# Optimization experiments

Hardware: AMD Instinct MI355X
Metric: run time of the kernel (lower is better)

## Reference

```python
import jax, jax.numpy as jnp
import numpy as np

# DCNV3_YOLO config: inc==ouc=128 (no stem_conv), k=3, s=1, pad=autopad(3)=1, g=4, d=1, SiLU act
N, C, H, W = 4, 128, 96, 96
G = 4
GC = C // G          # group channels = 32
K = 3                # dcn kernel (also depthwise conv kernel)
PAD = 1
P = K * K            # sampling points per group
EPS = 1e-5


def setup_inputs() -> dict:
    key = jax.random.key(0)
    ks = jax.random.split(key, 8)
    d = {}
    d["x"] = jax.random.normal(ks[0], (N, C, H, W), jnp.float32)
    # DCNv3 params (torch Linear weight (out,in) -> stored transposed (in,out) here)
    d["dw_w"] = jax.random.normal(ks[1], (C, 1, K, K), jnp.float32) * 0.1  # depthwise conv
    d["dw_b"] = jnp.zeros((C,), jnp.float32)
    d["ln_g"] = jnp.ones((C,), jnp.float32)   # LN inside dw_conv branch
    d["ln_b"] = jnp.zeros((C,), jnp.float32)
    d["w_off"] = jax.random.normal(ks[2], (C, G * P * 2), jnp.float32) * 0.01
    d["b_off"] = jnp.zeros((G * P * 2,), jnp.float32)
    d["w_mask"] = jax.random.normal(ks[3], (C, G * P), jnp.float32) * 0.02
    d["b_mask"] = jnp.zeros((G * P,), jnp.float32)
    d["w_in"] = jax.random.normal(ks[4], (C, C), jnp.float32) * (1.0 / np.sqrt(C))
    d["b_in"] = jnp.zeros((C,), jnp.float32)
    d["w_out"] = jax.random.normal(ks[5], (C, C), jnp.float32) * (1.0 / np.sqrt(C))
    d["b_out"] = jnp.zeros((C,), jnp.float32)
    # BatchNorm2d (eval mode: running stats)
    d["bn_g"] = jnp.ones((C,), jnp.float32)
    d["bn_b"] = jnp.zeros((C,), jnp.float32)
    d["bn_mean"] = jnp.zeros((C,), jnp.float32)
    d["bn_var"] = jnp.ones((C,), jnp.float32)
    return d


def _dcnv3_core(xp, offset, mask):
    # xp: (N,H,W,C) projected input; offset: (N,H,W,G*P*2); mask: (N,H,W,G,P) softmaxed
    n, h, w, _ = xp.shape
    xpad = jnp.pad(xp, ((0, 0), (PAD, PAD), (PAD, PAD), (0, 0)))
    H_in, W_in = h + 2 * PAD, w + 2 * PAD
    Ho, Wo = h, w  # stride 1, k=3, pad=1 -> same spatial size
    # reference points (pixel centers in padded frame, normalized), matches _get_reference_points
    base = (K - 1) // 2 + 0.5  # 1.5
    ref_y = (jnp.arange(Ho, dtype=jnp.float32) + base) / H_in
    ref_x = (jnp.arange(Wo, dtype=jnp.float32) + base) / W_in
    # dilation grid; torch flattens meshgrid(x_lin, y_lin) ij -> x outer, y inner
    lin = jnp.arange(K, dtype=jnp.float32) - (K - 1) // 2  # [-1,0,1]
    gx, gy = jnp.meshgrid(lin, lin, indexing='ij')  # (K,K), x varies along axis 0
    gridx = (gx / W_in).reshape(P)
    gridy = (gy / H_in).reshape(P)
    off = offset.reshape(n, Ho, Wo, G, P, 2)
    # normalized sampling locations (offset_scale = 1.0)
    loc_x = ref_x[None, None, :, None, None] + gridx[None, None, None, None, :] + off[..., 0] / W_in
    loc_y = ref_y[None, :, None, None, None] + gridy[None, None, None, None, :] + off[..., 1] / H_in
    # grid_sample(align_corners=False) unnormalize of (2*loc-1): loc*size - 0.5
    ix = (loc_x * W_in - 0.5).transpose(0, 3, 1, 2, 4)  # (N,G,Ho,Wo,P)
    iy = (loc_y * H_in - 0.5).transpose(0, 3, 1, 2, 4)
    x0 = jnp.floor(ix); y0 = jnp.floor(iy)
    wx1 = ix - x0; wx0 = 1.0 - wx1
    wy1 = iy - y0; wy0 = 1.0 - wy1
    x0i = x0.astype(jnp.int32); y0i = y0.astype(jnp.int32)
    x1i = x0i + 1; y1i = y0i + 1
    img = xpad.reshape(n, H_in * W_in, G, GC).transpose(0, 2, 1, 3)  # (N,G,S,GC)

    def samp(yi, xi, wgt):
        valid = (yi >= 0) & (yi < H_in) & (xi >= 0) & (xi < W_in)  # zeros padding
        idx = jnp.clip(yi, 0, H_in - 1) * W_in + jnp.clip(xi, 0, W_in - 1)
        idxf = idx.reshape(n, G, Ho * Wo * P, 1)
        v = jnp.take_along_axis(img, idxf, axis=2)  # (N,G,Ho*Wo*P,GC)
        w_eff = jnp.where(valid, wgt, 0.0).reshape(n, G, Ho * Wo * P, 1)
        return v * w_eff

    val = (samp(y0i, x0i, wy0 * wx0) + samp(y0i, x1i, wy0 * wx1)
           + samp(y1i, x0i, wy1 * wx0) + samp(y1i, x1i, wy1 * wx1))
    val = val.reshape(n, G, Ho, Wo, P, GC)
    m = mask.transpose(0, 3, 1, 2, 4)[..., None]  # (N,G,Ho,Wo,P,1)
    out = (val * m).sum(axis=4)  # (N,G,Ho,Wo,GC)
    return out.transpose(0, 2, 3, 1, 4).reshape(n, Ho, Wo, G * GC)


def reference(x, dw_w, dw_b, ln_g, ln_b, w_off, b_off, w_mask, b_mask,
              w_in, b_in, w_out, b_out, bn_g, bn_b, bn_mean, bn_var):
    x_nhwc = x.transpose(0, 2, 3, 1)  # NCHW -> NHWC
    x_proj = x_nhwc @ w_in + b_in     # input_proj
    # dw_conv branch: depthwise conv -> LayerNorm(channels_last) -> GELU
    x1 = jax.lax.conv_general_dilated(x, dw_w, (1, 1), ((PAD, PAD), (PAD, PAD)),
                                      feature_group_count=C,
                                      dimension_numbers=('NCHW', 'OIHW', 'NCHW'))
    x1 = x1.transpose(0, 2, 3, 1) + dw_b
    mu = x1.mean(-1, keepdims=True)
    var = ((x1 - mu) ** 2).mean(-1, keepdims=True)
    x1 = (x1 - mu) * jax.lax.rsqrt(var + EPS) * ln_g + ln_b
    x1 = jax.nn.gelu(x1, approximate=False)
    offset = x1 @ w_off + b_off  # (N,H,W,G*P*2)
    mask = jax.nn.softmax((x1 @ w_mask + b_mask).reshape(N, H, W, G, P), axis=-1)
    out = _dcnv3_core(x_proj, offset, mask)
    out = out @ w_out + b_out    # output_proj
    y = out.transpose(0, 3, 1, 2)  # back to NCHW
    # BatchNorm2d (eval) + SiLU
    inv = jax.lax.rsqrt(bn_var + EPS)
    y = (y - bn_mean[:, None, None]) * (inv * bn_g)[:, None, None] + bn_b[:, None, None]
    return y * jax.nn.sigmoid(y)
```

## Files before the change

### kernel.cpp

```cpp
#include <hip/hip_runtime.h>
#include <math.h>

#define NN 4
#define CCH 128
#define HH 96
#define WW 96
#define SS (HH*WW)
#define GG 4
#define GC 32
#define PP 9
#define NPIX (NN*HH*WW)

typedef short bf16x8 __attribute__((ext_vector_type(8)));
typedef float f32x4 __attribute__((ext_vector_type(4)));
typedef unsigned short u16;
typedef unsigned int u32;

static __device__ __forceinline__ u16 f2bf(float f) {
  unsigned u = __builtin_bit_cast(unsigned, f);
  unsigned r = (u + 0x7fffu + ((u >> 16) & 1u)) >> 16;
  return (u16)r;
}
static __device__ __forceinline__ float bflo(u32 u) {
  return __builtin_bit_cast(float, u << 16);
}
static __device__ __forceinline__ float bfhi(u32 u) {
  return __builtin_bit_cast(float, u & 0xffff0000u);
}

__global__ __launch_bounds__(128) void k_prep(const float* __restrict__ w_in,
    const float* __restrict__ w_off, const float* __restrict__ w_mask,
    const float* __restrict__ w_out, const float* __restrict__ dw_w,
    u16* __restrict__ w_inT, u16* __restrict__ w_omT, u16* __restrict__ w_outT,
    u16* __restrict__ dw_wT) {
  int r = blockIdx.x, k = threadIdx.x;
  if (r < 128) {
    w_inT[r*128 + k] = f2bf(w_in[k*128 + r]);
  } else if (r < 240) {
    int c = r - 128;
    float v = 0.f;
    if (c < 72) v = w_off[k*72 + c];
    else if (c < 108) v = w_mask[k*36 + (c - 72)];
    w_omT[c*128 + k] = f2bf(v);
  } else if (r < 368) {
    int c = r - 240;
    w_outT[c*128 + k] = f2bf(w_out[k*128 + c]);
  } else {
    int j = r - 368;
    dw_wT[j*128 + k] = f2bf(dw_w[k*9 + j]);
  }
}

__global__ __launch_bounds__(256) void k_trproj(const float* __restrict__ x,
    const u16* __restrict__ wT, const float* __restrict__ bias,
    u16* __restrict__ xTb, u16* __restrict__ xpb) {
  __shared__ u16 tile[32][136];
  int t = threadIdx.x;
  int pb = blockIdx.x * 32;
  int n = pb / SS, ps = pb % SS;
  const float* src = x + ((size_t)n*CCH)*SS + ps;

  #pragma unroll
  for (int i = 0; i < 4; ++i) {
    int fid = t + i*256;
    int c = fid >> 3, q = fid & 7;
    float4 v = *(const float4*)(src + (size_t)c*SS + q*4);
    int px = q*4;
    tile[px+0][c] = f2bf(v.x);
    tile[px+1][c] = f2bf(v.y);
    tile[px+2][c] = f2bf(v.z);
    tile[px+3][c] = f2bf(v.w);
  }
  __syncthreads();

  {
    u32* dst = (u32*)(xTb + (size_t)pb*CCH);
    #pragma unroll
    for (int i = 0; i < 8; ++i) {
      int gidx = t + i*256;
      int px = gidx >> 6, cp = gidx & 63;
      dst[(size_t)px*64 + cp] = *(const u32*)&tile[px][cp*2];
    }
  }

  {
    int wv = t >> 6, l = t & 63, c16 = l & 15, kq = l >> 4;
    int pxl0 = (wv & 1) * 16;
    int nt0 = (wv >> 1) * 4;
    bf16x8 a[4];
    #pragma unroll
    for (int ks = 0; ks < 4; ++ks)
      a[ks] = *(const bf16x8*)&tile[pxl0 + c16][kq*8 + ks*32];
    f32x4 acc[4] = {};
    #pragma unroll
    for (int ks = 0; ks < 4; ++ks) {
      #pragma unroll
      for (int j = 0; j < 4; ++j) {
        bf16x8 b = *(const bf16x8*)(wT + (size_t)((nt0+j)*16 + c16)*CCH + ks*32 + kq*8);
        acc[j] = __builtin_amdgcn_mfma_f32_16x16x32_bf16(a[ks], b, acc[j], 0, 0, 0);
      }
    }
    #pragma unroll
    for (int j = 0; j < 4; ++j) {
      int c = (nt0+j)*16 + c16;
      float bs = bias[c];
      #pragma unroll
      for (int r = 0; r < 4; ++r)
        xpb[(size_t)(pb + pxl0 + kq*4 + r)*CCH + c] = f2bf(acc[j][r] + bs);
    }
  }
}

__global__ __launch_bounds__(256) void k_dwom(const u16* __restrict__ xTb,
    const u16* __restrict__ dw_wT, const float* __restrict__ dw_b,
    const float* __restrict__ ln_g, const float* __restrict__ ln_b,
    const u16* __restrict__ wTom, const float* __restrict__ b_off,
    const float* __restrict__ b_mask,
    float* __restrict__ off, float* __restrict__ mask) {
  __shared__ u16 x1t[16][136];
  __shared__ float msk[16][40];
  int t = threadIdx.x;
  int blk = blockIdx.x;
  const int W16 = WW/16;
  int w0 = (blk % W16) * 16;
  int h  = (blk / W16) % HH;
  int n  = blk / (W16*HH);
  size_t pix0 = (size_t)n*SS + (size_t)h*WW + w0;

  {
    int px = t >> 4, cg = t & 15;
    int w = w0 + px;
    int c0 = cg * 8;
    const u16* src = xTb + (size_t)n*SS*CCH + c0;
    float wtv[9][8];
    #pragma unroll
    for (int j = 0; j < 9; ++j) {
      bf16x8 wr = *(const bf16x8*)(dw_wT + j*CCH + c0);
      u32 uw[4]; *(bf16x8*)uw = wr;
      #pragma unroll
      for (int q = 0; q < 4; ++q) { wtv[j][2*q] = bflo(uw[q]); wtv[j][2*q+1] = bfhi(uw[q]); }
    }
    float s8[8] = {};
    #pragma unroll
    for (int kh = 0; kh < 3; ++kh) {
      int yy = h - 1 + kh;
      if (yy < 0 || yy >= HH) continue;
      #pragma unroll
      for (int kw = 0; kw < 3; ++kw) {
        int xx = w - 1 + kw;
        if (xx < 0 || xx >= WW) continue;
        bf16x8 raw = *(const bf16x8*)(src + (size_t)(yy*WW + xx)*CCH);
        u32 uw[4]; *(bf16x8*)uw = raw;
        #pragma unroll
        for (int q = 0; q < 4; ++q) {
          s8[2*q]   = fmaf(bflo(uw[q]), wtv[kh*3+kw][2*q],   s8[2*q]);
          s8[2*q+1] = fmaf(bfhi(uw[q]), wtv[kh*3+kw][2*q+1], s8[2*q+1]);
        }
      }
    }
    float4 db0 = *(const float4*)(dw_b + c0);
    float4 db1 = *(const float4*)(dw_b + c0 + 4);
    s8[0]+=db0.x; s8[1]+=db0.y; s8[2]+=db0.z; s8[3]+=db0.w;
    s8[4]+=db1.x; s8[5]+=db1.y; s8[6]+=db1.z; s8[7]+=db1.w;
    float s1 = 0.f, s2 = 0.f;
    #pragma unroll
    for (int j = 0; j < 8; ++j) { s1 += s8[j]; s2 += s8[j]*s8[j]; }
    #pragma unroll
    for (int m = 8; m >= 1; m >>= 1) {
      s1 += __shfl_xor(s1, m);
      s2 += __shfl_xor(s2, m);
    }
    float mean = s1 * (1.f/128.f);
    float var  = s2 * (1.f/128.f) - mean*mean;
    float rstd = rsqrtf(var + 1e-5f);
    float4 lg0 = *(const float4*)(ln_g + c0);
    float4 lg1 = *(const float4*)(ln_g + c0 + 4);
    float4 lb0 = *(const float4*)(ln_b + c0);
    float4 lb1 = *(const float4*)(ln_b + c0 + 4);
    float lg[8] = {lg0.x,lg0.y,lg0.z,lg0.w,lg1.x,lg1.y,lg1.z,lg1.w};
    float lb[8] = {lb0.x,lb0.y,lb0.z,lb0.w,lb1.x,lb1.y,lb1.z,lb1.w};
    u32 pk[4];
    #pragma unroll
    for (int q = 0; q < 4; ++q) {
      float v0 = (s8[2*q]   - mean) * rstd * lg[2*q]   + lb[2*q];
      float v1 = (s8[2*q+1] - mean) * rstd * lg[2*q+1] + lb[2*q+1];
      float g0 = 0.5f * v0 * (1.f + erff(v0 * 0.70710678f));
      float g1 = 0.5f * v1 * (1.f + erff(v1 * 0.70710678f));
      pk[q] = (u32)f2bf(g0) | ((u32)f2bf(g1) << 16);
    }
    *(bf16x8*)&x1t[px][c0] = *(bf16x8*)pk;
  }
  __syncthreads();

  {
    int wv = t >> 6, l = t & 63, c16 = l & 15, kq = l >> 4;
    int nt0 = wv*2;
    int ntn = (wv == 3) ? 1 : 2;
    f32x4 acc[2] = {};
    #pragma unroll
    for (int ks = 0; ks < 4; ++ks) {
      bf16x8 a = *(const bf16x8*)&x1t[c16][kq*8 + ks*32];
      #pragma unroll
      for (int j = 0; j < 2; ++j) {
        if (j < ntn) {
          bf16x8 b = *(const bf16x8*)(wTom + (size_t)((nt0+j)*16 + c16)*CCH + ks*32 + kq*8);
          acc[j] = __builtin_amdgcn_mfma_f32_16x16x32_bf16(a, b, acc[j], 0, 0, 0);
        }
      }
    }
    #pragma unroll
    for (int j = 0; j < 2; ++j) {
      if (j < ntn) {
        int c = (nt0+j)*16 + c16;
        float bs = (c < 72) ? b_off[c] : ((c < 108) ? b_mask[c - 72] : 0.f);
        #pragma unroll
        for (int r = 0; r < 4; ++r) {
          int px = kq*4 + r;
          float v = acc[j][r] + bs;
          if (c < 72) off[(pix0 + px)*72 + c] = v;
          else if (c < 108) msk[px][c - 72] = v;
        }
      }
    }
  }
  __syncthreads();

  if (t < 64) {
    int px = t >> 2, g = t & 3;
    float mx = -1e30f;
    #pragma unroll
    for (int q = 0; q < PP; ++q) mx = fmaxf(mx, msk[px][g*PP + q]);
    float e[PP]; float sum = 0.f;
    #pragma unroll
    for (int q = 0; q < PP; ++q) { e[q] = __expf(msk[px][g*PP + q] - mx); sum += e[q]; }
    float inv = 1.f / sum;
    #pragma unroll
    for (int q = 0; q < PP; ++q)
      mask[(pix0 + px)*36 + g*PP + q] = e[q] * inv;
  }
}

__global__ __launch_bounds__(256) void k_dcnout(const u16* __restrict__ xpb,
    const float* __restrict__ off, const float* __restrict__ mask,
    const u16* __restrict__ wTout, const float* __restrict__ b_out,
    const float* __restrict__ bn_g, const float* __restrict__ bn_b,
    const float* __restrict__ bn_mean, const float* __restrict__ bn_var,
    float* __restrict__ y) {
  __shared__ float smem[16*132];
  __shared__ u16 dtile[16][136];
  float (*offs)[72] = (float(*)[72])smem;
  float (*ms)[36]   = (float(*)[36])(smem + 16*72);
  int t = threadIdx.x;
  int pb = blockIdx.x * 16;
  {
    const float* po = off + (size_t)pb*72;
    #pragma unroll
    for (int i = 0; i < 5; ++i) {
      int idx = t + i*256;
      if (idx < 16*72) smem[idx] = po[idx];
    }
    const float* pm = mask + (size_t)pb*36;
    #pragma unroll
    for (int i = 0; i < 3; ++i) {
      int idx = t + i*256;
      if (idx < 16*36) smem[16*72 + idx] = pm[idx];
    }
  }
  __syncthreads();

  {
    int pxl = t >> 4, unit = t & 15;
    int g = unit >> 2, ch0 = unit * 8;
    int pix = pb + pxl;
    int w = pix % WW; int h = (pix / WW) % HH; int n = pix / SS;
    const u16* basep = xpb + (size_t)n*SS*CCH + ch0;
    float a8[8] = {};
    #pragma unroll
    for (int bt = 0; bt < 3; ++bt) {
      bf16x8 raw[3][4];
      float wgt[3][4];
      #pragma unroll
      for (int q = 0; q < 3; ++q) {
        int p = bt*3 + q;
        float offx = offs[pxl][(g*PP + p)*2 + 0];
        float offy = offs[pxl][(g*PP + p)*2 + 1];
        float mval = ms[pxl][g*PP + p];
        float ix = (float)w + 1.0f + (float)(p / 3 - 1) + offx;
        float iy = (float)h + 1.0f + (float)(p % 3 - 1) + offy;
        float x0f = floorf(ix), y0f = floorf(iy);
        float wx1 = ix - x0f, wx0 = 1.f - wx1;
        float wy1 = iy - y0f, wy0 = 1.f - wy1;
        int x0i = (int)x0f, y0i = (int)y0f;
        int ox0 = x0i - 1, oy0 = y0i - 1;
        int ox1 = x0i,     oy1 = y0i;
        bool y0ok = (oy0 >= 0) & (oy0 < HH), y1ok = (oy1 >= 0) & (oy1 < HH);
        bool x0ok = (ox0 >= 0) & (ox0 < WW), x1ok = (ox1 >= 0) & (ox1 < WW);
        int cy0 = min(max(oy0, 0), HH-1), cy1 = min(max(oy1, 0), HH-1);
        int cx0 = min(max(ox0, 0), WW-1), cx1 = min(max(ox1, 0), WW-1);
        wgt[q][0] = ((y0ok & x0ok) ? wy0*wx0 : 0.f) * mval;
        wgt[q][1] = ((y0ok & x1ok) ? wy0*wx1 : 0.f) * mval;
        wgt[q][2] = ((y1ok & x0ok) ? wy1*wx0 : 0.f) * mval;
        wgt[q][3] = ((y1ok & x1ok) ? wy1*wx1 : 0.f) * mval;
        raw[q][0] = *(const bf16x8*)(basep + (size_t)(cy0*WW + cx0)*CCH);
        raw[q][1] = *(const bf16x8*)(basep + (size_t)(cy0*WW + cx1)*CCH);
        raw[q][2] = *(const bf16x8*)(basep + (size_t)(cy1*WW + cx0)*CCH);
        raw[q][3] = *(const bf16x8*)(basep + (size_t)(cy1*WW + cx1)*CCH);
      }
      #pragma unroll
      for (int q = 0; q < 3; ++q) {
        #pragma unroll
        for (int corner = 0; corner < 4; ++corner) {
          u32 uw[4]; *(bf16x8*)uw = raw[q][corner];
          float wg = wgt[q][corner];
          #pragma unroll
          for (int j = 0; j < 4; ++j) {
            a8[2*j]   = fmaf(wg, bflo(uw[j]), a8[2*j]);
            a8[2*j+1] = fmaf(wg, bfhi(uw[j]), a8[2*j+1]);
          }
        }
      }
    }
    u32 pk[4];
    #pragma unroll
    for (int j = 0; j < 4; ++j)
      pk[j] = (u32)f2bf(a8[2*j]) | ((u32)f2bf(a8[2*j+1]) << 16);
    *(bf16x8*)&dtile[pxl][ch0] = *(bf16x8*)pk;
  }
  __syncthreads();

  {
    int wv = t >> 6, l = t & 63, c16 = l & 15, kq = l >> 4;
    f32x4 acc[2] = {};
    #pragma unroll
    for (int ks = 0; ks < 4; ++ks) {
      bf16x8 a = *(const bf16x8*)&dtile[c16][kq*8 + ks*32];
      #pragma unroll
      for (int j = 0; j < 2; ++j) {
        int nt = wv*2 + j;
        bf16x8 b = *(const bf16x8*)(wTout + (size_t)(nt*16 + c16)*CCH + ks*32 + kq*8);
        acc[j] = __builtin_amdgcn_mfma_f32_16x16x32_bf16(a, b, acc[j], 0, 0, 0);
      }
    }
    float (*fout)[132] = (float(*)[132])smem;
    #pragma unroll
    for (int j = 0; j < 2; ++j) {
      int c = (wv*2 + j)*16 + c16;
      float sc = rsqrtf(bn_var[c] + 1e-5f) * bn_g[c];
      float sh = bn_b[c] - bn_mean[c] * sc;
      float bs = b_out[c];
      #pragma unroll
      for (int r = 0; r < 4; ++r) {
        int px = kq*4 + r;
        float v = (acc[j][r] + bs) * sc + sh;
        float sig = 1.f / (1.f + __expf(-v));
        fout[px][c] = v * sig;
      }
    }
  }
  __syncthreads();

  {
    float (*fout)[132] = (float(*)[132])smem;
    int n = pb / SS, rem = pb % SS;
    float* dst = y + ((size_t)n*CCH)*SS + rem;
    #pragma unroll
    for (int i = 0; i < 2; ++i) {
      int id = t + i*256;
      int c = id >> 2, p4 = (id & 3) * 4;
      float4 v = { fout[p4][c], fout[p4+1][c], fout[p4+2][c], fout[p4+3][c] };
      *(float4*)(dst + (size_t)c*SS + p4) = v;
    }
  }
}

extern "C" void kernel_launch(void* const* d_in, const int* in_sizes, int n_in,
                              void* d_out, int out_size, void* d_ws, size_t ws_size,
                              hipStream_t stream) {
  const float* x       = (const float*)d_in[0];
  const float* dw_w    = (const float*)d_in[1];
  const float* dw_b    = (const float*)d_in[2];
  const float* ln_g    = (const float*)d_in[3];
  const float* ln_b    = (const float*)d_in[4];
  const float* w_off   = (const float*)d_in[5];
  const float* b_off   = (const float*)d_in[6];
  const float* w_mask  = (const float*)d_in[7];
  const float* b_mask  = (const float*)d_in[8];
  const float* w_in    = (const float*)d_in[9];
  const float* b_in    = (const float*)d_in[10];
  const float* w_out   = (const float*)d_in[11];
  const float* b_out   = (const float*)d_in[12];
  const float* bn_g    = (const float*)d_in[13];
  const float* bn_b    = (const float*)d_in[14];
  const float* bn_mean = (const float*)d_in[15];
  const float* bn_var  = (const float*)d_in[16];
  float* y = (float*)d_out;

  u16*  xTb  = (u16*)d_ws;
  u16*  xpb  = xTb + (size_t)NPIX*CCH;
  float* offb = (float*)(xpb + (size_t)NPIX*CCH);
  float* mb   = offb + (size_t)NPIX*72;
  u16*  wbuf  = (u16*)(mb + (size_t)NPIX*36);
  u16*  w_inT  = wbuf;
  u16*  w_omT  = w_inT + 128*128;
  u16*  w_outT = w_omT + 112*128;
  u16*  dw_wTb = w_outT + 128*128;

  k_prep<<<377, 128, 0, stream>>>(w_in, w_off, w_mask, w_out, dw_w,
                                  w_inT, w_omT, w_outT, dw_wTb);
  k_trproj<<<NPIX/32, 256, 0, stream>>>(x, w_inT, b_in, xTb, xpb);
  k_dwom<<<NPIX/16, 256, 0, stream>>>(xTb, dw_wTb, dw_b, ln_g, ln_b,
                                      w_omT, b_off, b_mask, offb, mb);
  k_dcnout<<<NPIX/16, 256, 0, stream>>>(xpb, offb, mb, w_outT, b_out,
                                        bn_g, bn_b, bn_mean, bn_var, y);
}
```

Measured before the change: 171.9 us.

## Fuse offset/mask generation kernel with deformable sampling and output projection

Merges the depthwise-conv/LN/GELU/offset-mask kernel with the deformable sampling and output-projection kernel into one launch. Offsets and softmaxed masks now stay in shared memory per 16-pixel tile instead of going through global memory. This removes a kernel launch and the offset/mask round trip of about 108 floats per pixel. In exchange the fused kernel uses more registers and LDS, which may lower occupancy.

```diff
diff --git a/kernel.cpp b/kernel.cpp
--- a/kernel.cpp
+++ b/kernel.cpp
@@ -111,14 +111,19 @@
   }
 }
 
-__global__ __launch_bounds__(256) void k_dwom(const u16* __restrict__ xTb,
+__global__ __launch_bounds__(256) void k_dwomdcn(const u16* __restrict__ xTb,
+    const u16* __restrict__ xpb,
     const u16* __restrict__ dw_wT, const float* __restrict__ dw_b,
     const float* __restrict__ ln_g, const float* __restrict__ ln_b,
     const u16* __restrict__ wTom, const float* __restrict__ b_off,
     const float* __restrict__ b_mask,
-    float* __restrict__ off, float* __restrict__ mask) {
+    const u16* __restrict__ wTout, const float* __restrict__ b_out,
+    const float* __restrict__ bn_g, const float* __restrict__ bn_b,
+    const float* __restrict__ bn_mean, const float* __restrict__ bn_var,
+    float* __restrict__ y) {
   __shared__ u16 x1t[16][136];
-  __shared__ float msk[16][40];
+  __shared__ u16 dtile[16][136];
+  __shared__ float fbuf[16][132];
   int t = threadIdx.x;
   int blk = blockIdx.x;
   const int W16 = WW/16;
@@ -216,9 +221,7 @@
         #pragma unroll
         for (int r = 0; r < 4; ++r) {
           int px = kq*4 + r;
-          float v = acc[j][r] + bs;
-          if (c < 72) off[(pix0 + px)*72 + c] = v;
-          else if (c < 108) msk[px][c - 72] = v;
+          if (c < 108) fbuf[px][c] = acc[j][r] + bs;
         }
       }
     }
@@ -229,50 +232,20 @@
     int px = t >> 2, g = t & 3;
     float mx = -1e30f;
     #pragma unroll
-    for (int q = 0; q < PP; ++q) mx = fmaxf(mx, msk[px][g*PP + q]);
+    for (int q = 0; q < PP; ++q) mx = fmaxf(mx, fbuf[px][72 + g*PP + q]);
     float e[PP]; float sum = 0.f;
     #pragma unroll
-    for (int q = 0; q < PP; ++q) { e[q] = __expf(msk[px][g*PP + q] - mx); sum += e[q]; }
+    for (int q = 0; q < PP; ++q) { e[q] = __expf(fbuf[px][72 + g*PP + q] - mx); sum += e[q]; }
     float inv = 1.f / sum;
     #pragma unroll
-    for (int q = 0; q < PP; ++q)
-      mask[(pix0 + px)*36 + g*PP + q] = e[q] * inv;
-  }
-}
-
-__global__ __launch_bounds__(256) void k_dcnout(const u16* __restrict__ xpb,
-    const float* __restrict__ off, const float* __restrict__ mask,
-    const u16* __restrict__ wTout, const float* __restrict__ b_out,
-    const float* __restrict__ bn_g, const float* __restrict__ bn_b,
-    const float* __restrict__ bn_mean, const float* __restrict__ bn_var,
-    float* __restrict__ y) {
-  __shared__ float smem[16*132];
-  __shared__ u16 dtile[16][136];
-  float (*offs)[72] = (float(*)[72])smem;
-  float (*ms)[36]   = (float(*)[36])(smem + 16*72);
-  int t = threadIdx.x;
-  int pb = blockIdx.x * 16;
-  {
-    const float* po = off + (size_t)pb*72;
-    #pragma unroll
-    for (int i = 0; i < 5; ++i) {
-      int idx = t + i*256;
-      if (idx < 16*72) smem[idx] = po[idx];
-    }
-    const float* pm = mask + (size_t)pb*36;
-    #pragma unroll
-    for (int i = 0; i < 3; ++i) {
-      int idx = t + i*256;
-      if (idx < 16*36) smem[16*72 + idx] = pm[idx];
-    }
+    for (int q = 0; q < PP; ++q) fbuf[px][72 + g*PP + q] = e[q] * inv;
   }
   __syncthreads();
 
   {
     int pxl = t >> 4, unit = t & 15;
     int g = unit >> 2, ch0 = unit * 8;
-    int pix = pb + pxl;
-    int w = pix % WW; int h = (pix / WW) % HH; int n = pix / SS;
+    int w = w0 + pxl;
     const u16* basep = xpb + (size_t)n*SS*CCH + ch0;
     float a8[8] = {};
     #pragma unroll
@@ -282,9 +255,9 @@
       #pragma unroll
       for (int q = 0; q < 3; ++q) {
         int p = bt*3 + q;
-        float offx = offs[pxl][(g*PP + p)*2 + 0];
-        float offy = offs[pxl][(g*PP + p)*2 + 1];
-        float mval = ms[pxl][g*PP + p];
+        float offx = fbuf[pxl][(g*PP + p)*2 + 0];
+        float offy = fbuf[pxl][(g*PP + p)*2 + 1];
+        float mval = fbuf[pxl][72 + g*PP + p];
         float ix = (float)w + 1.0f + (float)(p / 3 - 1) + offx;
         float iy = (float)h + 1.0f + (float)(p % 3 - 1) + offy;
         float x0f = floorf(ix), y0f = floorf(iy);
@@ -341,7 +314,6 @@
         acc[j] = __builtin_amdgcn_mfma_f32_16x16x32_bf16(a, b, acc[j], 0, 0, 0);
       }
     }
-    float (*fout)[132] = (float(*)[132])smem;
     #pragma unroll
     for (int j = 0; j < 2; ++j) {
       int c = (wv*2 + j)*16 + c16;
@@ -353,21 +325,19 @@
         int px = kq*4 + r;
         float v = (acc[j][r] + bs) * sc + sh;
         float sig = 1.f / (1.f + __expf(-v));
-        fout[px][c] = v * sig;
-      }
-    }
-  }
-  __syncthreads();
-
-  {
-    float (*fout)[132] = (float(*)[132])smem;
-    int n = pb / SS, rem = pb % SS;
-    float* dst = y + ((size_t)n*CCH)*SS + rem;
+        fbuf[px][c] = v * sig;
+      }
+    }
+  }
+  __syncthreads();
+
+  {
+    float* dst = y + ((size_t)n*CCH)*SS + (size_t)h*WW + w0;
     #pragma unroll
     for (int i = 0; i < 2; ++i) {
       int id = t + i*256;
       int c = id >> 2, p4 = (id & 3) * 4;
-      float4 v = { fout[p4][c], fout[p4+1][c], fout[p4+2][c], fout[p4+3][c] };
+      float4 v = { fbuf[p4][c], fbuf[p4+1][c], fbuf[p4+2][c], fbuf[p4+3][c] };
       *(float4*)(dst + (size_t)c*SS + p4) = v;
     }
   }
@@ -397,9 +367,7 @@
 
   u16*  xTb  = (u16*)d_ws;
   u16*  xpb  = xTb + (size_t)NPIX*CCH;
-  float* offb = (float*)(xpb + (size_t)NPIX*CCH);
-  float* mb   = offb + (size_t)NPIX*72;
-  u16*  wbuf  = (u16*)(mb + (size_t)NPIX*36);
+  u16*  wbuf = xpb + (size_t)NPIX*CCH;
   u16*  w_inT  = wbuf;
   u16*  w_omT  = w_inT + 128*128;
   u16*  w_outT = w_omT + 112*128;
@@ -408,8 +376,8 @@
   k_prep<<<377, 128, 0, stream>>>(w_in, w_off, w_mask, w_out, dw_w,
                                   w_inT, w_omT, w_outT, dw_wTb);
   k_trproj<<<NPIX/32, 256, 0, stream>>>(x, w_inT, b_in, xTb, xpb);
-  k_dwom<<<NPIX/16, 256, 0, stream>>>(xTb, dw_wTb, dw_b, ln_g, ln_b,
-                                      w_omT, b_off, b_mask, offb, mb);
-  k_dcnout<<<NPIX/16, 256, 0, stream>>>(xpb, offb, mb, w_outT, b_out,
-                                        bn_g, bn_b, bn_mean, bn_var, y);
-}
+  k_dwomdcn<<<NPIX/16, 256, 0, stream>>>(xTb, xpb, dw_wTb, dw_b, ln_g, ln_b,
+                                         w_omT, b_off, b_mask,
+                                         w_outT, b_out,
+                                         bn_g, bn_b, bn_mean, bn_var, y);
+}
```

After: 164.3 us. 4.4% less time.
